# Kernel optimization log

Hardware: AMD Instinct MI355X
Metric: run time of the kernel (lower is better)

## Reference

```python
import jax, jax.numpy as jnp
import numpy as np

N, D_IN, D_HID, D_OUT, E = 8192, 1024, 4096, 1024, 8

def setup_inputs() -> dict:
    key = jax.random.key(0)
    ks = jax.random.split(key, 5)
    s_in = 1.0 / np.sqrt(D_IN)
    s_hid = 1.0 / np.sqrt(D_HID)
    return {
        "x": jax.random.normal(ks[0], (N, D_IN), dtype=jnp.float32),
        "W1": jax.random.normal(ks[1], (E, D_IN, D_HID), dtype=jnp.float32) * s_in,
        "b1": jnp.zeros((E, D_HID), dtype=jnp.float32),
        "W2": jax.random.normal(ks[2], (E, D_HID, D_OUT), dtype=jnp.float32) * s_hid,
        "b2": jnp.zeros((E, D_OUT), dtype=jnp.float32),
        "Wg": jax.random.normal(ks[3], (D_IN, E), dtype=jnp.float32) * s_in,
        "bg": jnp.zeros((E,), dtype=jnp.float32),
        "k": 2,
    }

def reference(x, W1, b1, W2, b2, Wg, bg, k):
    # Gating: softmax over ALL experts, then mask to top-k and renormalize
    scores = x @ Wg + bg                      # [N, E]
    _, topk_idx = jax.lax.top_k(scores, k)    # [N, k]
    mask = jax.nn.one_hot(topk_idx, scores.shape[-1], dtype=scores.dtype).sum(-2)  # [N, E]
    w = jax.nn.softmax(scores, axis=-1) * mask
    w = w / (w.sum(-1, keepdims=True) + 1e-8)  # [N, E]
    # Dense compute-all-experts (faithful to torch.stack over experts)
    h = jax.nn.relu(jnp.einsum('ni,eih->enh', x, W1) + b1[:, None, :])  # [E, N, hid]
    outs = jnp.einsum('enh,eho->eno', h, W2) + b2[:, None, :]           # [E, N, out]
    # Weighted combine over experts
    return jnp.einsum('ne,eno->no', w, outs)   # [N, out]
```

## Files before the change

### kernel.cpp

```cpp
#include <hip/hip_runtime.h>
#include <hip/hip_bf16.h>
#include <stdint.h>

#define N_TOK 8192
#define DIN   1024
#define DHID  4096
#define DOUT  1024
#define NE    8

typedef __attribute__((ext_vector_type(8))) __bf16 bf16x8;
typedef __attribute__((ext_vector_type(4))) float  f32x4;

__device__ __forceinline__ unsigned short f2bfu(float f) {
    union { float f; unsigned u; } a; a.f = f;
    unsigned r = a.u + 0x7FFF + ((a.u >> 16) & 1);
    return (unsigned short)(r >> 16);
}

__device__ __forceinline__ void gload_lds16(const void* g, void* l) {
    __builtin_amdgcn_global_load_lds(
        (__attribute__((address_space(1))) void*)(void*)g,
        (__attribute__((address_space(3))) void*)l,
        16, 0, 0);
}

__global__ void cast_x_kernel(const float* __restrict__ in, unsigned short* __restrict__ out) {
    int i = blockIdx.x * blockDim.x + threadIdx.x;
    float4 v = ((const float4*)in)[i];
    ushort4 o;
    o.x = f2bfu(v.x); o.y = f2bfu(v.y); o.z = f2bfu(v.z); o.w = f2bfu(v.w);
    ((ushort4*)out)[i] = o;
}

__global__ void transpose_cast_kernel(const float* __restrict__ in, unsigned short* __restrict__ out,
                                      int R, int C) {
    __shared__ float t[32][33];
    const float* ine = in + (size_t)blockIdx.z * R * C;
    unsigned short* oute = out + (size_t)blockIdx.z * R * C;
    int c0 = blockIdx.x * 32, r0 = blockIdx.y * 32;
    int tx = threadIdx.x, ty = threadIdx.y;
    #pragma unroll
    for (int j = 0; j < 32; j += 8)
        t[ty + j][tx] = ine[(size_t)(r0 + ty + j) * C + c0 + tx];
    __syncthreads();
    #pragma unroll
    for (int j = 0; j < 32; j += 8)
        oute[(size_t)(c0 + ty + j) * R + r0 + tx] = f2bfu(t[tx][ty + j]);
}

__global__ void gate_kernel(const float* __restrict__ x, const float* __restrict__ Wg,
                            const float* __restrict__ bg, int* __restrict__ counts,
                            int* __restrict__ tok_list, int* __restrict__ slot_list,
                            float* __restrict__ wslot) {
    int wv = threadIdx.x >> 6, lane = threadIdx.x & 63;
    int n = blockIdx.x * 4 + wv;
    float acc[NE];
    #pragma unroll
    for (int e = 0; e < NE; e++) acc[e] = 0.f;
    const float* xr = x + (size_t)n * DIN;
    #pragma unroll 4
    for (int i = 0; i < DIN / 64; i++) {
        int d = i * 64 + lane;
        float xv = xr[d];
        const float4* wr = (const float4*)(Wg + (size_t)d * NE);
        float4 w0 = wr[0], w1 = wr[1];
        acc[0] += xv * w0.x; acc[1] += xv * w0.y; acc[2] += xv * w0.z; acc[3] += xv * w0.w;
        acc[4] += xv * w1.x; acc[5] += xv * w1.y; acc[6] += xv * w1.z; acc[7] += xv * w1.w;
    }
    #pragma unroll
    for (int off = 32; off; off >>= 1)
        #pragma unroll
        for (int e = 0; e < NE; e++) acc[e] += __shfl_down(acc[e], off);
    if (lane == 0) {
        float s[NE], p[NE];
        float mx = -1e30f;
        #pragma unroll
        for (int e = 0; e < NE; e++) { s[e] = acc[e] + bg[e]; mx = fmaxf(mx, s[e]); }
        float sum = 0.f;
        #pragma unroll
        for (int e = 0; e < NE; e++) { p[e] = expf(s[e] - mx); sum += p[e]; }
        float inv = 1.f / sum;
        int e0 = 0;
        #pragma unroll
        for (int e = 1; e < NE; e++) if (s[e] > s[e0]) e0 = e;
        int e1 = (e0 == 0) ? 1 : 0;
        #pragma unroll
        for (int e = 0; e < NE; e++) if (e != e0 && s[e] > s[e1]) e1 = e;
        float p0 = p[e0] * inv, p1 = p[e1] * inv;
        float rn = 1.f / (p0 + p1 + 1e-8f);
        int pos0 = atomicAdd(&counts[e0], 1);
        tok_list[e0 * N_TOK + pos0] = n; slot_list[e0 * N_TOK + pos0] = 2 * n;     wslot[e0 * N_TOK + pos0] = p0 * rn;
        int pos1 = atomicAdd(&counts[e1], 1);
        tok_list[e1 * N_TOK + pos1] = n; slot_list[e1 * N_TOK + pos1] = 2 * n + 1; wslot[e1 * N_TOK + pos1] = p1 * rn;
    }
}

template <int KDIM, int NDIM, bool IS_GEMM1>
__global__ __launch_bounds__(256, 2)
void moe_gemm(const unsigned short* __restrict__ Asrc, const unsigned short* __restrict__ Bt,
              const float* __restrict__ bias, unsigned short* __restrict__ Hdst,
              float* __restrict__ Odst, const int* __restrict__ counts,
              const int* __restrict__ tok_list, const int* __restrict__ slot_list,
              const float* __restrict__ wslot) {
    int e = blockIdx.z;
    int tile_m = blockIdx.y;
    int tile_n = blockIdx.x;
    int count = counts[e];
    if (tile_m * 128 >= count) return;

    __shared__ __align__(16) unsigned short As[128 * 64];
    __shared__ __align__(16) unsigned short Bs[128 * 64];
    __shared__ int rowid_s[128];
    __shared__ int outid_s[128];
    __shared__ float w_s[128];

    int tid = threadIdx.x;
    if (tid < 128) {
        int r = tile_m * 128 + tid;
        int rr = (r < count) ? r : tile_m * 128;
        int base = e * N_TOK + rr;
        if (IS_GEMM1) { rowid_s[tid] = tok_list[base]; outid_s[tid] = slot_list[base]; }
        else          { rowid_s[tid] = slot_list[base]; outid_s[tid] = tok_list[base]; w_s[tid] = wslot[base]; }
    }
    __syncthreads();

    int lane = tid & 63;
    int wv = tid >> 6;

    const unsigned short* aptr[4];
    const unsigned short* bptr[4];
    #pragma unroll
    for (int i = 0; i < 4; i++) {
        int c = wv * 4 + i;
        int row = c * 8 + (lane >> 3);
        aptr[i] = Asrc + (size_t)rowid_s[row] * KDIM + (lane & 7) * 8;
        bptr[i] = Bt + ((size_t)e * NDIM + tile_n * 128 + row) * KDIM + (lane & 7) * 8;
    }

    f32x4 acc[4][4];
    #pragma unroll
    for (int i = 0; i < 4; i++)
        #pragma unroll
        for (int j = 0; j < 4; j++) acc[i][j] = (f32x4){0.f, 0.f, 0.f, 0.f};

    int wm = (wv >> 1) * 64, wn = (wv & 1) * 64;
    int r16 = lane & 15, quad = lane >> 4;

    for (int kk = 0; kk < KDIM / 64; kk++) {
        #pragma unroll
        for (int i = 0; i < 4; i++) {
            gload_lds16(aptr[i] + kk * 64, (void*)(As + (wv * 4 + i) * 512));
            gload_lds16(bptr[i] + kk * 64, (void*)(Bs + (wv * 4 + i) * 512));
        }
        __syncthreads();
        #pragma unroll
        for (int kh = 0; kh < 2; kh++) {
            bf16x8 av[4], bv[4];
            #pragma unroll
            for (int i = 0; i < 4; i++)
                av[i] = *(const bf16x8*)(As + (wm + i * 16 + r16) * 64 + kh * 32 + quad * 8);
            #pragma unroll
            for (int j = 0; j < 4; j++)
                bv[j] = *(const bf16x8*)(Bs + (wn + j * 16 + r16) * 64 + kh * 32 + quad * 8);
            #pragma unroll
            for (int i = 0; i < 4; i++)
                #pragma unroll
                for (int j = 0; j < 4; j++)
                    acc[i][j] = __builtin_amdgcn_mfma_f32_16x16x32_bf16(av[i], bv[j], acc[i][j], 0, 0, 0);
        }
        __syncthreads();
    }

    #pragma unroll
    for (int i = 0; i < 4; i++) {
        #pragma unroll
        for (int reg = 0; reg < 4; reg++) {
            int r = wm + i * 16 + quad * 4 + reg;
            if (tile_m * 128 + r >= count) continue;
            #pragma unroll
            for (int j = 0; j < 4; j++) {
                int col = tile_n * 128 + wn + j * 16 + r16;
                float v = acc[i][j][reg] + bias[(size_t)e * NDIM + col];
                if (IS_GEMM1) {
                    v = fmaxf(v, 0.f);
                    Hdst[(size_t)outid_s[r] * NDIM + col] = f2bfu(v);
                } else {
                    atomicAdd(&Odst[(size_t)outid_s[r] * NDIM + col], w_s[r] * v);
                }
            }
        }
    }
}

extern "C" void kernel_launch(void* const* d_in, const int* in_sizes, int n_in,
                              void* d_out, int out_size, void* d_ws, size_t ws_size,
                              hipStream_t stream) {
    const float* x  = (const float*)d_in[0];
    const float* W1 = (const float*)d_in[1];
    const float* b1 = (const float*)d_in[2];
    const float* W2 = (const float*)d_in[3];
    const float* b2 = (const float*)d_in[4];
    const float* Wg = (const float*)d_in[5];
    const float* bg = (const float*)d_in[6];
    float* out = (float*)d_out;

    char* ws = (char*)d_ws;
    unsigned short* xb  = (unsigned short*)(ws + 0);
    unsigned short* w1t = (unsigned short*)(ws + 16777216);
    unsigned short* w2t = (unsigned short*)(ws + 83886080);
    unsigned short* h   = (unsigned short*)(ws + 150994944);
    int*   counts    = (int*)(ws + 285212672);
    int*   tok_list  = (int*)(ws + 285212928);
    int*   slot_list = (int*)(ws + 285475072);
    float* wslot     = (float*)(ws + 285737216);

    hipMemsetAsync(counts, 0, 256, stream);
    hipMemsetAsync(d_out, 0, (size_t)out_size * sizeof(float), stream);

    cast_x_kernel<<<(N_TOK * DIN / 4) / 256, 256, 0, stream>>>(x, xb);
    transpose_cast_kernel<<<dim3(DHID / 32, DIN / 32, NE), dim3(32, 8), 0, stream>>>(W1, w1t, DIN, DHID);
    transpose_cast_kernel<<<dim3(DOUT / 32, DHID / 32, NE), dim3(32, 8), 0, stream>>>(W2, w2t, DHID, DOUT);
    gate_kernel<<<N_TOK / 4, 256, 0, stream>>>(x, Wg, bg, counts, tok_list, slot_list, wslot);

    moe_gemm<DIN, DHID, true><<<dim3(DHID / 128, N_TOK / 128, NE), 256, 0, stream>>>(
        xb, w1t, b1, h, nullptr, counts, tok_list, slot_list, wslot);
    moe_gemm<DHID, DOUT, false><<<dim3(DOUT / 128, N_TOK / 128, NE), 256, 0, stream>>>(
        h, w2t, b2, nullptr, out, counts, tok_list, slot_list, wslot);
}
```

Measured before the change: 1.020 ms.

## Fuse x cast into gate, widen transpose tiles, swizzle LDS, raise occupancy

The separate cast of x to bf16 is dropped and folded into the gate kernel, which now reads x once as float4 and writes the bf16 copy while computing the scores. The weight transpose-cast kernel moves to 64x64 tiles with float4 loads and 16-byte bf16 stores. The GEMM's LDS layout is XOR-swizzled on the k-chunk index to avoid bank conflicts on the MFMA operand reads. Launch bounds go from 2 to 4 blocks per SM, which may force register spilling in exchange for higher occupancy.

```diff
diff --git a/kernel.cpp b/kernel.cpp
--- a/kernel.cpp
+++ b/kernel.cpp
@@ -10,6 +10,7 @@
 
 typedef __attribute__((ext_vector_type(8))) __bf16 bf16x8;
 typedef __attribute__((ext_vector_type(4))) float  f32x4;
+typedef __attribute__((ext_vector_type(8))) unsigned short u16x8;
 
 __device__ __forceinline__ unsigned short f2bfu(float f) {
     union { float f; unsigned u; } a; a.f = f;
@@ -24,48 +25,60 @@
         16, 0, 0);
 }
 
-__global__ void cast_x_kernel(const float* __restrict__ in, unsigned short* __restrict__ out) {
-    int i = blockIdx.x * blockDim.x + threadIdx.x;
-    float4 v = ((const float4*)in)[i];
-    ushort4 o;
-    o.x = f2bfu(v.x); o.y = f2bfu(v.y); o.z = f2bfu(v.z); o.w = f2bfu(v.w);
-    ((ushort4*)out)[i] = o;
-}
-
 __global__ void transpose_cast_kernel(const float* __restrict__ in, unsigned short* __restrict__ out,
                                       int R, int C) {
-    __shared__ float t[32][33];
-    const float* ine = in + (size_t)blockIdx.z * R * C;
-    unsigned short* oute = out + (size_t)blockIdx.z * R * C;
-    int c0 = blockIdx.x * 32, r0 = blockIdx.y * 32;
-    int tx = threadIdx.x, ty = threadIdx.y;
-    #pragma unroll
-    for (int j = 0; j < 32; j += 8)
-        t[ty + j][tx] = ine[(size_t)(r0 + ty + j) * C + c0 + tx];
+    __shared__ float t[64][65];
+    const size_t RC = (size_t)R * C;
+    const float* ine = in + (size_t)blockIdx.z * RC;
+    unsigned short* oute = out + (size_t)blockIdx.z * RC;
+    int c0 = blockIdx.x * 64, r0 = blockIdx.y * 64;
+    int tid = threadIdx.x;
+    #pragma unroll
+    for (int it = 0; it < 4; it++) {
+        int idx = it * 256 + tid;
+        int r = idx >> 4, cq = (idx & 15) * 4;
+        float4 v = *(const float4*)(ine + (size_t)(r0 + r) * C + c0 + cq);
+        t[r][cq] = v.x; t[r][cq + 1] = v.y; t[r][cq + 2] = v.z; t[r][cq + 3] = v.w;
+    }
     __syncthreads();
     #pragma unroll
-    for (int j = 0; j < 32; j += 8)
-        oute[(size_t)(c0 + ty + j) * R + r0 + tx] = f2bfu(t[tx][ty + j]);
+    for (int it = 0; it < 2; it++) {
+        int u = it * 256 + tid;
+        int c = u >> 3, g = (u & 7) * 8;
+        u16x8 o;
+        #pragma unroll
+        for (int v = 0; v < 8; v++) o[v] = f2bfu(t[g + v][c]);
+        *(u16x8*)(oute + (size_t)(c0 + c) * R + r0 + g) = o;
+    }
 }
 
 __global__ void gate_kernel(const float* __restrict__ x, const float* __restrict__ Wg,
                             const float* __restrict__ bg, int* __restrict__ counts,
                             int* __restrict__ tok_list, int* __restrict__ slot_list,
-                            float* __restrict__ wslot) {
+                            float* __restrict__ wslot, unsigned short* __restrict__ xb) {
     int wv = threadIdx.x >> 6, lane = threadIdx.x & 63;
     int n = blockIdx.x * 4 + wv;
     float acc[NE];
     #pragma unroll
     for (int e = 0; e < NE; e++) acc[e] = 0.f;
     const float* xr = x + (size_t)n * DIN;
-    #pragma unroll 4
-    for (int i = 0; i < DIN / 64; i++) {
-        int d = i * 64 + lane;
-        float xv = xr[d];
-        const float4* wr = (const float4*)(Wg + (size_t)d * NE);
-        float4 w0 = wr[0], w1 = wr[1];
-        acc[0] += xv * w0.x; acc[1] += xv * w0.y; acc[2] += xv * w0.z; acc[3] += xv * w0.w;
-        acc[4] += xv * w1.x; acc[5] += xv * w1.y; acc[6] += xv * w1.z; acc[7] += xv * w1.w;
+    unsigned short* xbr = xb + (size_t)n * DIN;
+    #pragma unroll
+    for (int i = 0; i < DIN / 256; i++) {
+        int d = i * 256 + lane * 4;
+        float4 xv = *(const float4*)(xr + d);
+        ushort4 o;
+        o.x = f2bfu(xv.x); o.y = f2bfu(xv.y); o.z = f2bfu(xv.z); o.w = f2bfu(xv.w);
+        *(ushort4*)(xbr + d) = o;
+        const float* w = Wg + (size_t)d * NE;
+        #pragma unroll
+        for (int u = 0; u < 4; u++) {
+            float xs = (&xv.x)[u];
+            float4 w0 = *(const float4*)(w + u * NE);
+            float4 w1 = *(const float4*)(w + u * NE + 4);
+            acc[0] += xs * w0.x; acc[1] += xs * w0.y; acc[2] += xs * w0.z; acc[3] += xs * w0.w;
+            acc[4] += xs * w1.x; acc[5] += xs * w1.y; acc[6] += xs * w1.z; acc[7] += xs * w1.w;
+        }
     }
     #pragma unroll
     for (int off = 32; off; off >>= 1)
@@ -96,7 +109,7 @@
 }
 
 template <int KDIM, int NDIM, bool IS_GEMM1>
-__global__ __launch_bounds__(256, 2)
+__global__ __launch_bounds__(256, 4)
 void moe_gemm(const unsigned short* __restrict__ Asrc, const unsigned short* __restrict__ Bt,
               const float* __restrict__ bias, unsigned short* __restrict__ Hdst,
               float* __restrict__ Odst, const int* __restrict__ counts,
@@ -127,14 +140,16 @@
     int lane = tid & 63;
     int wv = tid >> 6;
 
+    int ric = lane >> 3;
+    int k8  = (lane & 7) ^ ric;
     const unsigned short* aptr[4];
     const unsigned short* bptr[4];
     #pragma unroll
     for (int i = 0; i < 4; i++) {
         int c = wv * 4 + i;
-        int row = c * 8 + (lane >> 3);
-        aptr[i] = Asrc + (size_t)rowid_s[row] * KDIM + (lane & 7) * 8;
-        bptr[i] = Bt + ((size_t)e * NDIM + tile_n * 128 + row) * KDIM + (lane & 7) * 8;
+        int row = c * 8 + ric;
+        aptr[i] = Asrc + (size_t)rowid_s[row] * KDIM + k8 * 8;
+        bptr[i] = Bt + ((size_t)e * NDIM + tile_n * 128 + row) * KDIM + k8 * 8;
     }
 
     f32x4 acc[4][4];
@@ -155,13 +170,14 @@
         __syncthreads();
         #pragma unroll
         for (int kh = 0; kh < 2; kh++) {
+            int swk = ((kh * 4 + quad) ^ (r16 & 7)) * 8;
             bf16x8 av[4], bv[4];
             #pragma unroll
             for (int i = 0; i < 4; i++)
-                av[i] = *(const bf16x8*)(As + (wm + i * 16 + r16) * 64 + kh * 32 + quad * 8);
+                av[i] = *(const bf16x8*)(As + (wm + i * 16 + r16) * 64 + swk);
             #pragma unroll
             for (int j = 0; j < 4; j++)
-                bv[j] = *(const bf16x8*)(Bs + (wn + j * 16 + r16) * 64 + kh * 32 + quad * 8);
+                bv[j] = *(const bf16x8*)(Bs + (wn + j * 16 + r16) * 64 + swk);
             #pragma unroll
             for (int i = 0; i < 4; i++)
                 #pragma unroll
@@ -217,10 +233,9 @@
     hipMemsetAsync(counts, 0, 256, stream);
     hipMemsetAsync(d_out, 0, (size_t)out_size * sizeof(float), stream);
 
-    cast_x_kernel<<<(N_TOK * DIN / 4) / 256, 256, 0, stream>>>(x, xb);
-    transpose_cast_kernel<<<dim3(DHID / 32, DIN / 32, NE), dim3(32, 8), 0, stream>>>(W1, w1t, DIN, DHID);
-    transpose_cast_kernel<<<dim3(DOUT / 32, DHID / 32, NE), dim3(32, 8), 0, stream>>>(W2, w2t, DHID, DOUT);
-    gate_kernel<<<N_TOK / 4, 256, 0, stream>>>(x, Wg, bg, counts, tok_list, slot_list, wslot);
+    transpose_cast_kernel<<<dim3(DHID / 64, DIN / 64, NE), 256, 0, stream>>>(W1, w1t, DIN, DHID);
+    transpose_cast_kernel<<<dim3(DOUT / 64, DHID / 64, NE), 256, 0, stream>>>(W2, w2t, DHID, DOUT);
+    gate_kernel<<<N_TOK / 4, 256, 0, stream>>>(x, Wg, bg, counts, tok_list, slot_list, wslot, xb);
 
     moe_gemm<DIN, DHID, true><<<dim3(DHID / 128, N_TOK / 128, NE), 256, 0, stream>>>(
         xb, w1t, b1, h, nullptr, counts, tok_list, slot_list, wslot);
```

Result: faster. 953.1 us (-6.6%).
